# Performance work log

Measured on AMD Instinct MI355X. Metric: run time of the kernel, lower is better.

## Reference

```python
import math
import jax, jax.numpy as jnp
import numpy as np

NUM_CODE = 4096
CODE_DIM = 256
IN_DIM = 1024

def chi_dist_mean_std(c):
    mean = math.sqrt(2.0) * math.exp(math.lgamma((c + 1) / 2) - math.lgamma(c / 2))
    std = math.sqrt(c - mean ** 2)
    return mean, std

MU, SIGMA = chi_dist_mean_std(CODE_DIM)


def setup_inputs() -> dict:
    key = jax.random.key(0)
    k1, k2, k3 = jax.random.split(key, 3)
    encode = jax.random.normal(k1, (8, 64, 64, CODE_DIM), dtype=jnp.float32)
    codebook_w = jax.random.normal(k2, (NUM_CODE, IN_DIM), dtype=jnp.float32)  # N(0,1) init
    proj_w = jax.random.normal(k3, (CODE_DIM, IN_DIM), dtype=jnp.float32) * (1.0 / math.sqrt(IN_DIM))
    proj_b = jnp.zeros((CODE_DIM,), dtype=jnp.float32)
    return {"encode": encode, "codebook_w": codebook_w, "proj_w": proj_w, "proj_b": proj_b}


def _cdist(z, e):
    # pairwise euclidean distance: [T, K]
    z2 = jnp.sum(z * z, axis=-1, keepdims=True)          # [T,1]
    e2 = jnp.sum(e * e, axis=-1)[None, :]                # [1,K]
    d2 = z2 + e2 - 2.0 * jnp.einsum('tc,kc->tk', z, e)
    return jnp.sqrt(jnp.maximum(d2, 0.0))


def reference(encode, codebook_w, proj_w, proj_b):
    b, h, w, c = encode.shape
    e = codebook_w @ proj_w.T + proj_b                   # [K, code_dim]
    z = encode.reshape(-1, c)                            # [T, code_dim]
    s = -_cdist(z, e)                                    # [T, K] (computed under no_grad in torch)
    simi = (s.reshape(b, h, w, -1) - MU) / SIGMA
    zsoft = jax.nn.softmax(simi, axis=-1)                # eval path (std=0)
    zidx = jnp.argmax(zsoft, axis=-1)                    # [b,h,w]
    quant = e[zidx]                                      # [b,h,w,code_dim]
    return (zidx, quant)
```

## Files before the change

kernel.cpp:

```cpp
#include <hip/hip_runtime.h>
#include <hip/hip_bf16.h>


#define K_CODES 4096
#define CDIM    256
#define IDIM    1024
#define NTOK    32768

typedef __attribute__((ext_vector_type(8))) short short8;
typedef __attribute__((ext_vector_type(4))) float f32x4;

__device__ __forceinline__ unsigned short f32_to_bf16_rne(float f) {
  union { float f; unsigned int u; } x; x.f = f;
  unsigned int r = x.u + 0x7FFFu + ((x.u >> 16) & 1u);
  return (unsigned short)(r >> 16);
}
__device__ __forceinline__ float bf16_to_f32(unsigned short h) {
  union { unsigned int u; float f; } x; x.u = ((unsigned int)h) << 16;
  return x.f;
}

extern "C" __global__ __launch_bounds__(256)
void proj_gemm(const float* __restrict__ cb, const float* __restrict__ pw,
               const float* __restrict__ pb, float* __restrict__ e,
               unsigned short* __restrict__ Ect) {
  __shared__ float As[32][68];
  __shared__ float Bs[32][68];
  const int tid = threadIdx.x;
  const int tx = tid & 15, ty = tid >> 4;
  const int m0 = blockIdx.y << 6;
  const int n0 = blockIdx.x << 6;
  const int r  = tid >> 2;
  const int c8 = (tid & 3) << 3;
  float acc[4][4] = {};
  for (int k0 = 0; k0 < IDIM; k0 += 32) {
    float4 a0 = *(const float4*)&cb[(m0 + r) * IDIM + k0 + c8];
    float4 a1 = *(const float4*)&cb[(m0 + r) * IDIM + k0 + c8 + 4];
    float4 b0 = *(const float4*)&pw[(n0 + r) * IDIM + k0 + c8];
    float4 b1 = *(const float4*)&pw[(n0 + r) * IDIM + k0 + c8 + 4];
    __syncthreads();
    As[c8+0][r]=a0.x; As[c8+1][r]=a0.y; As[c8+2][r]=a0.z; As[c8+3][r]=a0.w;
    As[c8+4][r]=a1.x; As[c8+5][r]=a1.y; As[c8+6][r]=a1.z; As[c8+7][r]=a1.w;
    Bs[c8+0][r]=b0.x; Bs[c8+1][r]=b0.y; Bs[c8+2][r]=b0.z; Bs[c8+3][r]=b0.w;
    Bs[c8+4][r]=b1.x; Bs[c8+5][r]=b1.y; Bs[c8+6][r]=b1.z; Bs[c8+7][r]=b1.w;
    __syncthreads();
    #pragma unroll
    for (int kk = 0; kk < 32; ++kk) {
      const float4 av = *(const float4*)&As[kk][ty*4];
      const float4 bv = *(const float4*)&Bs[kk][tx*4];
      const float a4[4] = {av.x, av.y, av.z, av.w};
      const float b4[4] = {bv.x, bv.y, bv.z, bv.w};
      #pragma unroll
      for (int i = 0; i < 4; ++i)
        #pragma unroll
        for (int j = 0; j < 4; ++j)
          acc[i][j] += a4[i] * b4[j];
    }
  }
  const int col0 = n0 + tx*4;
  const int kb   = col0 >> 5;
  const int g    = (col0 >> 3) & 3;
  const int half = (col0 >> 2) & 1;
  #pragma unroll
  for (int i = 0; i < 4; ++i) {
    const int row = m0 + ty*4 + i;
    float vv[4];
    unsigned short h4[4], l4[4];
    #pragma unroll
    for (int j = 0; j < 4; ++j) {
      vv[j] = acc[i][j] + pb[col0 + j];
      h4[j] = f32_to_bf16_rne(vv[j]);
      l4[j] = f32_to_bf16_rne(vv[j] - bf16_to_f32(h4[j]));
    }
    *(float4*)&e[(size_t)row * CDIM + col0] = *(float4*)vv;
    const int ct = row >> 4, cl = row & 15;
    const size_t fi = ((size_t)(kb      * 256 + ct) * 64 + g*16 + cl) * 8 + half*4;
    const size_t fo = ((size_t)((kb+8)  * 256 + ct) * 64 + g*16 + cl) * 8 + half*4;
    *(ushort4*)&Ect[fi] = *(ushort4*)h4;
    *(ushort4*)&Ect[fo] = *(ushort4*)l4;
  }
}

extern "C" __global__ __launch_bounds__(256)
void compute_e2(const float* __restrict__ e, float* __restrict__ e2) {
  const int gid  = blockIdx.x * 256 + threadIdx.x;
  const int w    = gid >> 6;
  const int lane = threadIdx.x & 63;
  float4 v = *(const float4*)&e[(size_t)w * CDIM + (lane << 2)];
  float s = v.x*v.x + v.y*v.y + v.z*v.z + v.w*v.w;
  #pragma unroll
  for (int off = 32; off > 0; off >>= 1) s += __shfl_down(s, off, 64);
  if (lane == 0) e2[w] = s;
}

extern "C" __global__ __launch_bounds__(512, 2)
void score_mfma(const float* __restrict__ z, const unsigned short* __restrict__ Ect,
                const float* __restrict__ e2g, const float* __restrict__ eg,
                float* __restrict__ zidx_f, float* __restrict__ quant) {
  extern __shared__ __align__(16) char smem[];
  char* Zb = smem;

  const int tid = threadIdx.x;
  const int l   = tid & 63;
  const int w   = tid >> 6;
  const int tg  = w >> 2;
  const int cg  = w & 3;
  const int t0  = blockIdx.x << 7;

  #pragma unroll
  for (int rr = 0; rr < 2; ++rr) {
    const int r  = rr*64 + (tid >> 3);
    const int cq = tid & 7;
    const int i8 = r >> 4;
    const int rl = (r & 15) << 4;
    #pragma unroll
    for (int it = 0; it < 4; ++it) {
      const int col = cq*32 + it*8;
      const float4 v0 = *(const float4*)&z[(size_t)(t0 + r) * CDIM + col];
      const float4 v1 = *(const float4*)&z[(size_t)(t0 + r) * CDIM + col + 4];
      float vv[8] = {v0.x,v0.y,v0.z,v0.w,v1.x,v1.y,v1.z,v1.w};
      unsigned int hp[4], lp[4];
      #pragma unroll
      for (int c = 0; c < 4; ++c) {
        unsigned short h0 = f32_to_bf16_rne(vv[2*c]);
        unsigned short h1 = f32_to_bf16_rne(vv[2*c+1]);
        unsigned short l0 = f32_to_bf16_rne(vv[2*c]   - bf16_to_f32(h0));
        unsigned short l1 = f32_to_bf16_rne(vv[2*c+1] - bf16_to_f32(h1));
        hp[c] = (unsigned int)h0 | ((unsigned int)h1 << 16);
        lp[c] = (unsigned int)l0 | ((unsigned int)l1 << 16);
      }
      const int lane_b = it*256 + rl;
      *(uint4*)(Zb + (size_t)(i8*16 + cq    ) * 1024 + lane_b) = *(uint4*)hp;
      *(uint4*)(Zb + (size_t)(i8*16 + cq + 8) * 1024 + lane_b) = *(uint4*)lp;
    }
  }
  __syncthreads();

  float bestv[4][4];
  int   besti[4][4];
  #pragma unroll
  for (int i = 0; i < 4; ++i)
    #pragma unroll
    for (int r = 0; r < 4; ++r) { bestv[i][r] = 3.4e38f; besti[i][r] = 0; }

  const int cl = l & 15;
  const int g  = l >> 4;

  const char* ebase = (const char*)Ect + (size_t)l * 16 + (size_t)cg * 4096;
  const char* Zl    = Zb + (size_t)l * 16 + (size_t)tg * 65536;

  short8 aHc[4], aLc[4], bHc[4], bLc[4];
  #pragma unroll
  for (int i = 0; i < 4; ++i) {
    aHc[i] = *(const short8*)(Zl + (size_t)(i*16 + 0) * 1024);
    aLc[i] = *(const short8*)(Zl + (size_t)(i*16 + 8) * 1024);
  }
  #pragma unroll
  for (int jj = 0; jj < 4; ++jj) {
    bHc[jj] = *(const short8*)(ebase + (size_t)0 * 262144 + jj * 1024);
    bLc[jj] = *(const short8*)(ebase + (size_t)8 * 262144 + jj * 1024);
  }

  for (int cc = 0; cc < 16; ++cc) {
    const char* ecc  = ebase + (size_t)cc * 16384;
    const char* eccn = ebase + (size_t)((cc + 1) & 15) * 16384;

    f32x4 acc[4][4];
    #pragma unroll
    for (int i = 0; i < 4; ++i)
      #pragma unroll
      for (int jj = 0; jj < 4; ++jj) acc[i][jj] = (f32x4){0.f,0.f,0.f,0.f};

    float e2v[4];
    #pragma unroll
    for (int jj = 0; jj < 4; ++jj)
      e2v[jj] = e2g[cc*256 + cg*64 + jj*16 + cl];

    #pragma unroll
    for (int kw = 0; kw < 8; ++kw) {
      short8 aHn[4], aLn[4], bHn[4], bLn[4];
      {
        const char* bsrc = (kw < 7) ? ecc : eccn;
        const int kwn = (kw + 1) & 7;
        #pragma unroll
        for (int jj = 0; jj < 4; ++jj) {
          bHn[jj] = *(const short8*)(bsrc + (size_t)(kwn    ) * 262144 + jj * 1024);
          bLn[jj] = *(const short8*)(bsrc + (size_t)(kwn + 8) * 262144 + jj * 1024);
        }
        #pragma unroll
        for (int i = 0; i < 4; ++i) {
          aHn[i] = *(const short8*)(Zl + (size_t)(i*16 + kwn    ) * 1024);
          aLn[i] = *(const short8*)(Zl + (size_t)(i*16 + kwn + 8) * 1024);
        }
      }
      __builtin_amdgcn_s_setprio(1);
      #pragma unroll
      for (int i = 0; i < 4; ++i)
        #pragma unroll
        for (int jj = 0; jj < 4; ++jj)
          acc[i][jj] = __builtin_amdgcn_mfma_f32_16x16x32_bf16(aHc[i], bHc[jj], acc[i][jj], 0, 0, 0);
      #pragma unroll
      for (int i = 0; i < 4; ++i)
        #pragma unroll
        for (int jj = 0; jj < 4; ++jj)
          acc[i][jj] = __builtin_amdgcn_mfma_f32_16x16x32_bf16(aHc[i], bLc[jj], acc[i][jj], 0, 0, 0);
      #pragma unroll
      for (int i = 0; i < 4; ++i)
        #pragma unroll
        for (int jj = 0; jj < 4; ++jj)
          acc[i][jj] = __builtin_amdgcn_mfma_f32_16x16x32_bf16(aLc[i], bHc[jj], acc[i][jj], 0, 0, 0);
      __builtin_amdgcn_s_setprio(0);
      #pragma unroll
      for (int i = 0; i < 4; ++i) { aHc[i] = aHn[i]; aLc[i] = aLn[i]; }
      #pragma unroll
      for (int jj = 0; jj < 4; ++jj) { bHc[jj] = bHn[jj]; bLc[jj] = bLn[jj]; }
    }
    #pragma unroll
    for (int jj = 0; jj < 4; ++jj) {
      const int code = cc*256 + cg*64 + jj*16 + cl;
      #pragma unroll
      for (int i = 0; i < 4; ++i)
        #pragma unroll
        for (int r = 0; r < 4; ++r) {
          const float sc = e2v[jj] - 2.0f * acc[i][jj][r];
          if (sc < bestv[i][r]) { bestv[i][r] = sc; besti[i][r] = code; }
        }
    }
  }

  struct RP { float v; int i; };
  RP*  red    = (RP*)(smem + 131072);
  int* sh_idx = (int*)(smem + 131072 + 4096);
  #pragma unroll
  for (int i = 0; i < 4; ++i)
    #pragma unroll
    for (int r = 0; r < 4; ++r) {
      float v = bestv[i][r]; int bi = besti[i][r];
      #pragma unroll
      for (int m = 1; m < 16; m <<= 1) {
        const float ov = __shfl_xor(v, m, 64);
        const int   oi = __shfl_xor(bi, m, 64);
        if (ov < v || (ov == v && oi < bi)) { v = ov; bi = oi; }
      }
      if (cl == 0) {
        const int tl = tg*64 + i*16 + g*4 + r;
        red[tl*4 + cg].v = v; red[tl*4 + cg].i = bi;
      }
    }
  __syncthreads();
  if (tid < 128) {
    float v = red[tid*4].v; int bi = red[tid*4].i;
    #pragma unroll
    for (int x = 1; x < 4; ++x) {
      const float ov = red[tid*4 + x].v; const int oi = red[tid*4 + x].i;
      if (ov < v || (ov == v && oi < bi)) { v = ov; bi = oi; }
    }
    zidx_f[t0 + tid] = (float)bi;
    sh_idx[tid] = bi;
  }
  __syncthreads();

  #pragma unroll
  for (int rr = 0; rr < 2; ++rr) {
    const int r   = rr*64 + (tid >> 3);
    const int cq  = (tid & 7) << 5;
    const int idx = sh_idx[r];
    #pragma unroll
    for (int it = 0; it < 4; ++it) {
      const float4 v0 = *(const float4*)&eg[(size_t)idx * CDIM + cq + it*8];
      const float4 v1 = *(const float4*)&eg[(size_t)idx * CDIM + cq + it*8 + 4];
      *(float4*)&quant[(size_t)(t0 + r) * CDIM + cq + it*8]     = v0;
      *(float4*)&quant[(size_t)(t0 + r) * CDIM + cq + it*8 + 4] = v1;
    }
  }
}

extern "C" void kernel_launch(void* const* d_in, const int* in_sizes, int n_in,
                              void* d_out, int out_size, void* d_ws, size_t ws_size,
                              hipStream_t stream) {
  const float* encode = (const float*)d_in[0];
  const float* cb     = (const float*)d_in[1];
  const float* pw     = (const float*)d_in[2];
  const float* pb     = (const float*)d_in[3];

  float* e  = (float*)d_ws;
  float* e2 = e + (size_t)K_CODES * CDIM;
  unsigned short* Ect = (unsigned short*)(e2 + K_CODES);

  float* out     = (float*)d_out;
  float* zidx_f  = out;
  float* quant_f = out + NTOK;

  (void)hipFuncSetAttribute((const void*)score_mfma,
                            hipFuncAttributeMaxDynamicSharedMemorySize, 135680);

  proj_gemm<<<dim3(CDIM/64, K_CODES/64), 256, 0, stream>>>(cb, pw, pb, e, Ect);
  compute_e2<<<(K_CODES*64)/256, 256, 0, stream>>>(e, e2);
  score_mfma<<<NTOK/128, 512, 135680, stream>>>(encode, Ect, e2, e, zidx_f, quant_f);
}
```

Baseline: 222.6 us.

## Fuse codebook squared-norm into projection GEMM epilogue, widen to 512 threads

Removes the separate compute_e2 launch. The projection GEMM epilogue now computes partial squared norms per 64-column block, reduces them with lane shuffles, and writes four partials per code. The score kernel sums these four partials when it loads e2. The projection kernel also moves to 512 threads per block with a 2x4 micro-tile instead of 4x4. This saves one launch and one pass over e, at the cost of four loads per code in the score kernel and a smaller per-thread tile.

```diff
diff --git a/kernel.cpp b/kernel.cpp
--- a/kernel.cpp
+++ b/kernel.cpp
@@ -20,50 +20,47 @@
   return x.f;
 }
 
-extern "C" __global__ __launch_bounds__(256)
+extern "C" __global__ __launch_bounds__(512)
 void proj_gemm(const float* __restrict__ cb, const float* __restrict__ pw,
                const float* __restrict__ pb, float* __restrict__ e,
-               unsigned short* __restrict__ Ect) {
+               unsigned short* __restrict__ Ect, float* __restrict__ e2p) {
   __shared__ float As[32][68];
   __shared__ float Bs[32][68];
   const int tid = threadIdx.x;
   const int tx = tid & 15, ty = tid >> 4;
   const int m0 = blockIdx.y << 6;
   const int n0 = blockIdx.x << 6;
-  const int r  = tid >> 2;
-  const int c8 = (tid & 3) << 3;
-  float acc[4][4] = {};
+  const int r  = tid >> 3;
+  const int c4 = (tid & 7) << 2;
+  float acc[2][4] = {};
   for (int k0 = 0; k0 < IDIM; k0 += 32) {
-    float4 a0 = *(const float4*)&cb[(m0 + r) * IDIM + k0 + c8];
-    float4 a1 = *(const float4*)&cb[(m0 + r) * IDIM + k0 + c8 + 4];
-    float4 b0 = *(const float4*)&pw[(n0 + r) * IDIM + k0 + c8];
-    float4 b1 = *(const float4*)&pw[(n0 + r) * IDIM + k0 + c8 + 4];
+    float4 a0 = *(const float4*)&cb[(size_t)(m0 + r) * IDIM + k0 + c4];
+    float4 b0 = *(const float4*)&pw[(size_t)(n0 + r) * IDIM + k0 + c4];
     __syncthreads();
-    As[c8+0][r]=a0.x; As[c8+1][r]=a0.y; As[c8+2][r]=a0.z; As[c8+3][r]=a0.w;
-    As[c8+4][r]=a1.x; As[c8+5][r]=a1.y; As[c8+6][r]=a1.z; As[c8+7][r]=a1.w;
-    Bs[c8+0][r]=b0.x; Bs[c8+1][r]=b0.y; Bs[c8+2][r]=b0.z; Bs[c8+3][r]=b0.w;
-    Bs[c8+4][r]=b1.x; Bs[c8+5][r]=b1.y; Bs[c8+6][r]=b1.z; Bs[c8+7][r]=b1.w;
+    As[c4+0][r]=a0.x; As[c4+1][r]=a0.y; As[c4+2][r]=a0.z; As[c4+3][r]=a0.w;
+    Bs[c4+0][r]=b0.x; Bs[c4+1][r]=b0.y; Bs[c4+2][r]=b0.z; Bs[c4+3][r]=b0.w;
     __syncthreads();
     #pragma unroll
     for (int kk = 0; kk < 32; ++kk) {
-      const float4 av = *(const float4*)&As[kk][ty*4];
+      const float2 av = *(const float2*)&As[kk][ty*2];
       const float4 bv = *(const float4*)&Bs[kk][tx*4];
-      const float a4[4] = {av.x, av.y, av.z, av.w};
+      const float a2[2] = {av.x, av.y};
       const float b4[4] = {bv.x, bv.y, bv.z, bv.w};
       #pragma unroll
-      for (int i = 0; i < 4; ++i)
+      for (int i = 0; i < 2; ++i)
         #pragma unroll
         for (int j = 0; j < 4; ++j)
-          acc[i][j] += a4[i] * b4[j];
+          acc[i][j] += a2[i] * b4[j];
     }
   }
   const int col0 = n0 + tx*4;
   const int kb   = col0 >> 5;
   const int g    = (col0 >> 3) & 3;
   const int half = (col0 >> 2) & 1;
-  #pragma unroll
-  for (int i = 0; i < 4; ++i) {
-    const int row = m0 + ty*4 + i;
+  float p2[2];
+  #pragma unroll
+  for (int i = 0; i < 2; ++i) {
+    const int row = m0 + ty*2 + i;
     float vv[4];
     unsigned short h4[4], l4[4];
     #pragma unroll
@@ -78,24 +75,22 @@
     const size_t fo = ((size_t)((kb+8)  * 256 + ct) * 64 + g*16 + cl) * 8 + half*4;
     *(ushort4*)&Ect[fi] = *(ushort4*)h4;
     *(ushort4*)&Ect[fo] = *(ushort4*)l4;
-  }
-}
-
-extern "C" __global__ __launch_bounds__(256)
-void compute_e2(const float* __restrict__ e, float* __restrict__ e2) {
-  const int gid  = blockIdx.x * 256 + threadIdx.x;
-  const int w    = gid >> 6;
-  const int lane = threadIdx.x & 63;
-  float4 v = *(const float4*)&e[(size_t)w * CDIM + (lane << 2)];
-  float s = v.x*v.x + v.y*v.y + v.z*v.z + v.w*v.w;
-  #pragma unroll
-  for (int off = 32; off > 0; off >>= 1) s += __shfl_down(s, off, 64);
-  if (lane == 0) e2[w] = s;
+    p2[i] = vv[0]*vv[0] + vv[1]*vv[1] + vv[2]*vv[2] + vv[3]*vv[3];
+  }
+  #pragma unroll
+  for (int m = 1; m < 16; m <<= 1) {
+    p2[0] += __shfl_xor(p2[0], m, 64);
+    p2[1] += __shfl_xor(p2[1], m, 64);
+  }
+  if (tx == 0) {
+    e2p[(size_t)blockIdx.x * K_CODES + m0 + ty*2    ] = p2[0];
+    e2p[(size_t)blockIdx.x * K_CODES + m0 + ty*2 + 1] = p2[1];
+  }
 }
 
 extern "C" __global__ __launch_bounds__(512, 2)
 void score_mfma(const float* __restrict__ z, const unsigned short* __restrict__ Ect,
-                const float* __restrict__ e2g, const float* __restrict__ eg,
+                const float* __restrict__ e2p, const float* __restrict__ eg,
                 float* __restrict__ zidx_f, float* __restrict__ quant) {
   extern __shared__ __align__(16) char smem[];
   char* Zb = smem;
@@ -173,8 +168,11 @@
 
     float e2v[4];
     #pragma unroll
-    for (int jj = 0; jj < 4; ++jj)
-      e2v[jj] = e2g[cc*256 + cg*64 + jj*16 + cl];
+    for (int jj = 0; jj < 4; ++jj) {
+      const int code = cc*256 + cg*64 + jj*16 + cl;
+      e2v[jj] = e2p[code] + e2p[K_CODES + code]
+              + e2p[2*K_CODES + code] + e2p[3*K_CODES + code];
+    }
 
     #pragma unroll
     for (int kw = 0; kw < 8; ++kw) {
@@ -283,9 +281,9 @@
   const float* pw     = (const float*)d_in[2];
   const float* pb     = (const float*)d_in[3];
 
-  float* e  = (float*)d_ws;
-  float* e2 = e + (size_t)K_CODES * CDIM;
-  unsigned short* Ect = (unsigned short*)(e2 + K_CODES);
+  float* e   = (float*)d_ws;
+  float* e2p = e + (size_t)K_CODES * CDIM;
+  unsigned short* Ect = (unsigned short*)(e2p + 4*K_CODES);
 
   float* out     = (float*)d_out;
   float* zidx_f  = out;
@@ -294,7 +292,6 @@
   (void)hipFuncSetAttribute((const void*)score_mfma,
                             hipFuncAttributeMaxDynamicSharedMemorySize, 135680);
 
-  proj_gemm<<<dim3(CDIM/64, K_CODES/64), 256, 0, stream>>>(cb, pw, pb, e, Ect);
-  compute_e2<<<(K_CODES*64)/256, 256, 0, stream>>>(e, e2);
-  score_mfma<<<NTOK/128, 512, 135680, stream>>>(encode, Ect, e2, e, zidx_f, quant_f);
-}
+  proj_gemm<<<dim3(CDIM/64, K_CODES/64), 512, 0, stream>>>(cb, pw, pb, e, Ect, e2p);
+  score_mfma<<<NTOK/128, 512, 135680, stream>>>(encode, Ect, e2p, e, zidx_f, quant_f);
+}
```

Measured after the change: 222.5 us. About the same (-0.1%).
